# Optimization experiments

Measured on AMD Instinct MI355X. Metric: run time of the kernel, lower is better.

## Reference

```python
import jax, jax.numpy as jnp
import numpy as np
import math
from jax import lax

BATCH, SEQ_LEN, ENC_IN = 8, 2048, 1
D_MODEL, N_HEADS, E_LAYERS, D_FF, FACTOR, C_OUT = 512, 8, 3, 512, 5, 2
EPS = 1e-5


def _layernorm(x, g, b):
    mu = x.mean(-1, keepdims=True)
    var = ((x - mu) ** 2).mean(-1, keepdims=True)
    return (x - mu) / jnp.sqrt(var + EPS) * g + b


def _prob_attention(q, k, v, key):
    # q,k,v: [B,H,L,Dh]; ProbSparse: sample U keys per query, pick top-u queries by M = max - mean
    B, H, L, Dh = q.shape
    U = min(FACTOR * int(np.ceil(np.log(L))), L)  # U_part == u since L_Q == L_K
    idx = jax.random.randint(key, (L, U), 0, L)   # sampled key indices per query
    k_samp = k[:, :, idx, :]                       # [B,H,L,U,Dh]
    qk = jnp.einsum('bhld,bhlud->bhlu', q, k_samp)
    M = qk.max(-1) - qk.mean(-1)                   # sparsity measure [B,H,L]
    _, top = lax.top_k(M, U)                       # active query indices [B,H,U]
    q_red = jnp.take_along_axis(q, top[..., None], axis=2)
    scores = jnp.einsum('bhud,bhkd->bhuk', q_red, k) * (1.0 / math.sqrt(Dh))
    A = jax.nn.softmax(scores, axis=-1)
    ctx = jnp.broadcast_to(v.mean(axis=2, keepdims=True), q.shape)  # lazy-query context = mean(V)
    upd = jnp.einsum('bhuk,bhkd->bhud', A, v)
    b = jnp.arange(B)[:, None, None]
    h = jnp.arange(H)[None, :, None]
    return ctx.at[b, h, top].set(upd)


def _encoder_layer(x, p, key):
    Wq, Wk, Wv, bq, bk, bv, Wo, bo, W1, b1, W2, b2, g1, be1, g2, be2 = p
    B, L, dm = x.shape
    Dh = dm // N_HEADS
    split = lambda t: t.reshape(B, L, N_HEADS, Dh).transpose(0, 2, 1, 3)
    q = split(x @ Wq.T + bq)
    k = split(x @ Wk.T + bk)
    v = split(x @ Wv.T + bv)
    o = _prob_attention(q, k, v, key).transpose(0, 2, 1, 3).reshape(B, L, dm)
    x = _layernorm(x + o @ Wo.T + bo, g1, be1)
    y = jax.nn.gelu(x @ W1.T + b1, approximate=False) @ W2.T + b2  # 1x1 convs == linears
    return _layernorm(x + y, g2, be2)


def _distil_conv(x, w, b, g, be):
    # Conv1d(dm,dm,3, circular pad) -> BatchNorm(eval) -> ELU -> MaxPool1d(3, stride 2, pad 1)
    xc = jnp.pad(x.transpose(0, 2, 1), ((0, 0), (0, 0), (1, 1)), mode='wrap')
    y = lax.conv_general_dilated(xc, w, (1,), 'VALID', dimension_numbers=('NCH', 'OIH', 'NCH'))
    y = y + b[None, :, None]
    y = y / np.float32(np.sqrt(1.0 + EPS)) * g[None, :, None] + be[None, :, None]
    y = jax.nn.elu(y)
    y = lax.reduce_window(y, -jnp.inf, lax.max, (1, 1, 3), (1, 1, 2), [(0, 0), (0, 0), (1, 1)])
    return y.transpose(0, 2, 1)


def _forward(x_enc, tok_w, Wq, Wk, Wv, bq, bk, bv, Wo, bo, W1, b1, W2, b2,
             ln1_g, ln1_b, ln2_g, ln2_b, dc_w, dc_b, bn_g, bn_b, lnf_g, lnf_b, proj_w, proj_b):
    B, L = x_enc.shape
    dm = D_MODEL
    # TokenEmbedding: circular Conv1d(1, d_model, 3, bias=False)
    xc = jnp.pad(x_enc[:, None, :], ((0, 0), (0, 0), (1, 1)), mode='wrap')
    tok = lax.conv_general_dilated(xc, tok_w, (1,), 'VALID', dimension_numbers=('NCH', 'OIH', 'NCH'))
    tok = tok.transpose(0, 2, 1)  # [B,L,dm]
    # fixed sinusoidal positional embedding
    pos = jnp.arange(L, dtype=jnp.float32)[:, None]
    div = jnp.exp(jnp.arange(0, dm, 2, dtype=jnp.float32) * (-math.log(10000.0) / dm))
    pe = jnp.zeros((L, dm), jnp.float32).at[:, 0::2].set(jnp.sin(pos * div)).at[:, 1::2].set(jnp.cos(pos * div))
    x = tok + pe[None]
    key = jax.random.key(42)
    for i in range(E_LAYERS):
        p = (Wq[i], Wk[i], Wv[i], bq[i], bk[i], bv[i], Wo[i], bo[i],
             W1[i], b1[i], W2[i], b2[i], ln1_g[i], ln1_b[i], ln2_g[i], ln2_b[i])
        x = _encoder_layer(x, p, jax.random.fold_in(key, i))
        if i < E_LAYERS - 1:
            x = _distil_conv(x, dc_w[i], dc_b[i], bn_g[i], bn_b[i])
    x = _layernorm(x, lnf_g, lnf_b)
    return x.max(axis=1) @ proj_w.T + proj_b  # [B, C_OUT]


def setup_inputs() -> dict:
    key = jax.random.key(0)
    ks = jax.random.split(key, 12)
    dm, dff, L = D_MODEL, D_FF, E_LAYERS
    w = lambda k, shape, fan: jax.random.normal(k, shape, jnp.float32) / np.float32(np.sqrt(fan))
    return {
        'x_enc': jax.random.normal(ks[0], (BATCH, SEQ_LEN), jnp.float32),
        'tok_w': w(ks[1], (dm, ENC_IN, 3), 3 * ENC_IN),
        'Wq': w(ks[2], (L, dm, dm), dm), 'Wk': w(ks[3], (L, dm, dm), dm),
        'Wv': w(ks[4], (L, dm, dm), dm), 'Wo': w(ks[5], (L, dm, dm), dm),
        'bq': jnp.zeros((L, dm)), 'bk': jnp.zeros((L, dm)),
        'bv': jnp.zeros((L, dm)), 'bo': jnp.zeros((L, dm)),
        'W1': w(ks[6], (L, dff, dm), dm), 'b1': jnp.zeros((L, dff)),
        'W2': w(ks[7], (L, dm, dff), dff), 'b2': jnp.zeros((L, dm)),
        'ln1_g': jnp.ones((L, dm)), 'ln1_b': jnp.zeros((L, dm)),
        'ln2_g': jnp.ones((L, dm)), 'ln2_b': jnp.zeros((L, dm)),
        'dc_w': w(ks[8], (L - 1, dm, dm, 3), 3 * dm), 'dc_b': jnp.zeros((L - 1, dm)),
        'bn_g': jnp.ones((L - 1, dm)), 'bn_b': jnp.zeros((L - 1, dm)),
        'lnf_g': jnp.ones((dm,)), 'lnf_b': jnp.zeros((dm,)),
        'proj_w': w(ks[9], (C_OUT, dm), dm), 'proj_b': jnp.zeros((C_OUT,)),
    }


def reference(x_enc, tok_w, Wq, Wk, Wv, bq, bk, bv, Wo, bo, W1, b1, W2, b2,
              ln1_g, ln1_b, ln2_g, ln2_b, dc_w, dc_b, bn_g, bn_b, lnf_g, lnf_b, proj_w, proj_b):
    return _forward(x_enc, tok_w, Wq, Wk, Wv, bq, bk, bv, Wo, bo, W1, b1, W2, b2,
                    ln1_g, ln1_b, ln2_g, ln2_b, dc_w, dc_b, bn_g, bn_b, lnf_g, lnf_b, proj_w, proj_b)
```

## Files before the change

### kernel.cpp

```cpp
#include <hip/hip_runtime.h>

#define B_ 8
#define H_ 8
#define DM 512
#define DH 64
#define LMAX 2048
#define COUT 2

typedef __attribute__((ext_vector_type(8))) short frag8;
typedef __attribute__((ext_vector_type(4))) float f32x4;

typedef __attribute__((address_space(1))) const unsigned int guint;
typedef __attribute__((address_space(3))) unsigned int luint;
__device__ __forceinline__ void dma16(const short* g, short* l) {
  __builtin_amdgcn_global_load_lds((guint*)g, (luint*)l, 16, 0, 0);
}

__device__ __forceinline__ short f2bf(float v) {
  unsigned u = __float_as_uint(v);
  unsigned r = (u + 0x7fffu + ((u >> 16) & 1u)) >> 16;
  return (short)r;
}
__device__ __forceinline__ float bf2f(short s) {
  return __uint_as_float(((unsigned)(unsigned short)s) << 16);
}
__device__ __forceinline__ void split3(float v, short* p0, short* p1, short* p2, size_t i) {
  short h0 = f2bf(v);
  float r1 = v - bf2f(h0);
  short h1 = f2bf(r1);
  float r2 = r1 - bf2f(h1);
  p0[i] = h0; p1[i] = h1; p2[i] = f2bf(r2);
}

__device__ __forceinline__ void tf2x32(unsigned k0, unsigned k1, unsigned x0, unsigned x1,
                                       unsigned& o0, unsigned& o1) {
  unsigned ks2 = k0 ^ k1 ^ 0x1BD11BDAu;
  x0 += k0; x1 += k1;
#define RND(r) { x0 += x1; x1 = (x1 << r) | (x1 >> (32 - r)); x1 ^= x0; }
  RND(13) RND(15) RND(26) RND(6)  x0 += k1;  x1 += ks2 + 1u;
  RND(17) RND(29) RND(16) RND(24) x0 += ks2; x1 += k0 + 2u;
  RND(13) RND(15) RND(26) RND(6)  x0 += k0;  x1 += k1 + 3u;
  RND(17) RND(29) RND(16) RND(24) x0 += k1;  x1 += ks2 + 4u;
  RND(13) RND(15) RND(26) RND(6)  x0 += ks2; x1 += k0 + 5u;
#undef RND
  o0 = x0; o1 = x1;
}

__global__ void idx_kernel(int* __restrict__ idxArr, int L, int U, int layer) {
  int p = blockIdx.x * 256 + threadIdx.x;
  int half = L * U;
  if (p >= half) return;
  unsigned fk0, fk1, k20, k21, o0, o1;
  tf2x32(0u, 42u, 0u, (unsigned)layer, fk0, fk1);
  tf2x32(fk0, fk1, 0u, 1u, k20, k21);
  tf2x32(k20, k21, 0u, (unsigned)p, o0, o1);
  idxArr[p] = (int)((o0 ^ o1) & (unsigned)(L - 1));
}

__global__ void embed_kernel(const float* __restrict__ xe, const float* __restrict__ tw,
                             float* __restrict__ X, short* __restrict__ P0,
                             short* __restrict__ P1, short* __restrict__ P2) {
  int i = blockIdx.x * 256 + threadIdx.x;
  int c = i % DM;
  int l = (i / DM) % LMAX;
  int b = i / (DM * LMAX);
  int lm = (l + LMAX - 1) & (LMAX - 1);
  int lp = (l + 1) & (LMAX - 1);
  const float* xb = xe + b * LMAX;
  float tok = tw[c * 3 + 0] * xb[lm] + tw[c * 3 + 1] * xb[l] + tw[c * 3 + 2] * xb[lp];
  float freq = expf(-(float)(c & ~1) * (9.210340371976184f / 512.0f));
  float ang = (float)l * freq;
  float pe = (c & 1) ? cosf(ang) : sinf(ang);
  float v = tok + pe;
  X[i] = v;
  split3(v, P0, P1, P2, (size_t)i);
}

__global__ void wsplit_kernel(const float* __restrict__ W, short* __restrict__ P0,
                              short* __restrict__ P1, short* __restrict__ P2, int n) {
  int i = blockIdx.x * 256 + threadIdx.x;
  if (i >= n) return;
  split3(W[i], P0, P1, P2, (size_t)i);
}

__global__ void wt3_kernel(const float* __restrict__ w, short* __restrict__ P0,
                           short* __restrict__ P1, short* __restrict__ P2) {
  int i = blockIdx.x * 256 + threadIdx.x;
  int n = i / 1536, r = i - n * 1536, tap = r >> 9, k = r & 511;
  float v = w[((size_t)n * DM + k) * 3 + tap];
  split3(v, P0, P1, P2, (size_t)i);
}

template <int ACT, int QKV, int ACC, int CONV>
__global__ __launch_bounds__(256) void mgemm(const short* __restrict__ A0g,
                                             const short* __restrict__ A1g,
                                             const short* __restrict__ A2g,
                                             const short* __restrict__ W0g,
                                             const short* __restrict__ W1g,
                                             const short* __restrict__ W2g,
                                             const float* __restrict__ bias,
                                             float* __restrict__ C, int L, int Ktot) {
  __shared__ short A0[128 * 32], A1[128 * 32], A2[128 * 32];
  __shared__ short B0[128 * 32], B1[128 * 32], B2[128 * 32];
  int tid = threadIdx.x;
  int lane = tid & 63, wave = tid >> 6;
  int crow = lane >> 2, ckq = lane & 3;
  int gx = gridDim.x;
  int flat = blockIdx.y * gx + blockIdx.x;
  int mB, nB;
  if ((gridDim.y & 7) == 0) {
    int phase = flat & 7, sup = flat >> 3;
    nB = sup % gx;
    mB = phase + 8 * (sup / gx);
  } else {
    nB = blockIdx.x; mB = blockIdx.y;
  }
  int n0 = nB * 128, m0 = mB * 128;
  int wm = (wave >> 1) * 64, wn = (wave & 1) * 64;
  f32x4 acc[4][4] = {};
  int lrow = lane & 15, lq = lane >> 4;

  for (int k0 = 0; k0 < Ktot; k0 += 32) {
    int tap = 0, kcol = k0;
    if (CONV) { tap = k0 >> 9; kcol = k0 & 511; }
#pragma unroll
    for (int q = 0; q < 6; ++q) {
      int gc = wave * 6 + q;
      int pl = gc >> 3, c = gc & 7;
      int grow = m0 + c * 16 + crow;
      const short* gp;
      if (CONV) {
        int b = grow / L, l = grow - b * L;
        int le = l + tap - 1;
        le = (le < 0) ? le + L : (le >= L ? le - L : le);
        gp = ((size_t)(b * L + le) * DM + kcol + ckq * 8) +
             (pl == 0 ? A0g : pl == 1 ? A1g : A2g);
      } else {
        gp = ((size_t)grow * DM + k0 + ckq * 8) +
             (pl == 0 ? A0g : pl == 1 ? A1g : A2g);
      }
      short* lp = (pl == 0 ? A0 : pl == 1 ? A1 : A2) + c * 512;
      dma16(gp, lp);
    }
#pragma unroll
    for (int q = 0; q < 6; ++q) {
      int gc = wave * 6 + q;
      int pl = gc >> 3, c = gc & 7;
      int grow = n0 + c * 16 + crow;
      const short* gp = ((size_t)grow * Ktot + k0 + ckq * 8) +
                        (pl == 0 ? W0g : pl == 1 ? W1g : W2g);
      short* lp = (pl == 0 ? B0 : pl == 1 ? B1 : B2) + c * 512;
      dma16(gp, lp);
    }
    __syncthreads();
    frag8 a0f[4], a1f[4], a2f[4];
#pragma unroll
    for (int ti = 0; ti < 4; ++ti) {
      int off = (wm + ti * 16 + lrow) * 32 + lq * 8;
      a0f[ti] = *(const frag8*)&A0[off];
      a1f[ti] = *(const frag8*)&A1[off];
      a2f[ti] = *(const frag8*)&A2[off];
    }
#pragma unroll
    for (int tj = 0; tj < 4; ++tj) {
      int off = (wn + tj * 16 + lrow) * 32 + lq * 8;
      frag8 b0 = *(const frag8*)&B0[off];
      frag8 b1 = *(const frag8*)&B1[off];
      frag8 b2 = *(const frag8*)&B2[off];
#pragma unroll
      for (int ti = 0; ti < 4; ++ti) {
        f32x4 ac = acc[ti][tj];
        ac = __builtin_amdgcn_mfma_f32_16x16x32_bf16(a1f[ti], b1, ac, 0, 0, 0);
        ac = __builtin_amdgcn_mfma_f32_16x16x32_bf16(a0f[ti], b2, ac, 0, 0, 0);
        ac = __builtin_amdgcn_mfma_f32_16x16x32_bf16(a2f[ti], b0, ac, 0, 0, 0);
        ac = __builtin_amdgcn_mfma_f32_16x16x32_bf16(a0f[ti], b1, ac, 0, 0, 0);
        ac = __builtin_amdgcn_mfma_f32_16x16x32_bf16(a1f[ti], b0, ac, 0, 0, 0);
        ac = __builtin_amdgcn_mfma_f32_16x16x32_bf16(a0f[ti], b0, ac, 0, 0, 0);
        acc[ti][tj] = ac;
      }
    }
    __syncthreads();
  }
#pragma unroll
  for (int ti = 0; ti < 4; ++ti) {
#pragma unroll
    for (int tj = 0; tj < 4; ++tj) {
#pragma unroll
      for (int r = 0; r < 4; ++r) {
        int row = m0 + wm + ti * 16 + lq * 4 + r;
        int col = n0 + wn + tj * 16 + lrow;
        float v = acc[ti][tj][r];
        if (!CONV) v += bias[col];
        if (ACT) v = 0.5f * v * (1.0f + erff(v * 0.70710678118654752f));
        if (QKV) {
          int b = row / L, l = row - b * L;
          int h = col >> 6, d = col & 63;
          C[(((size_t)b * H_ + h) * L + l) * DH + d] = v;
        } else if (ACC) {
          C[(size_t)row * DM + col] += v;
        } else {
          C[(size_t)row * DM + col] = v;
        }
      }
    }
  }
}

__global__ void bnelu_kernel(float* __restrict__ Y, const float* __restrict__ cb,
                             const float* __restrict__ g, const float* __restrict__ be) {
  int i = blockIdx.x * 256 + threadIdx.x;
  int c = i % DM;
  const float invs = 0.9999950000374997f;
  float z = Y[i] + cb[c];
  z = z * invs * g[c] + be[c];
  Y[i] = z > 0.f ? z : expm1f(z);
}

template <int U>
__global__ void qkM_t(const float* __restrict__ Q, const float* __restrict__ Kd,
                      const int* __restrict__ idxArr, float* __restrict__ Mout, int L) {
  int lane = threadIdx.x & 63, wv = threadIdx.x >> 6;
  int row = blockIdx.x * 4 + wv;
  int l = row % L, bh = row / L;
  int u = lane & 7, dc = lane >> 3;
  const float* Qb = Q + ((size_t)bh * L + l) * DH + dc * 8;
  float4 q0 = *(const float4*)(Qb);
  float4 q1 = *(const float4*)(Qb + 4);
  const float* Kb = Kd + (size_t)bh * L * DH;
  const int* ip = idxArr + l * U;
  const int NP = (U + 7) / 8;
  float mx = -1e30f, sm = 0.f;
#pragma unroll
  for (int p = 0; p < NP; ++p) {
    int s = p * 8 + u;
    bool valid = (s < U);
    int ki = ip[valid ? s : 0];
    const float* kr = Kb + (size_t)ki * DH + dc * 8;
    float4 k0 = *(const float4*)(kr);
    float4 k1 = *(const float4*)(kr + 4);
    float d = q0.x * k0.x + q0.y * k0.y + q0.z * k0.z + q0.w * k0.w +
              q1.x * k1.x + q1.y * k1.y + q1.z * k1.z + q1.w * k1.w;
    d += __shfl_xor(d, 8, 64);
    d += __shfl_xor(d, 16, 64);
    d += __shfl_xor(d, 32, 64);
    if (valid) { mx = fmaxf(mx, d); sm += d; }
  }
#pragma unroll
  for (int o = 1; o <= 4; o <<= 1) {
    mx = fmaxf(mx, __shfl_xor(mx, o, 64));
    sm += __shfl_xor(sm, o, 64);
  }
  if (lane == 0) Mout[row] = mx - sm / (float)U;
}

__global__ void topk_kernel(const float* __restrict__ M, int* __restrict__ top, int L, int U) {
  __shared__ float vals[LMAX];
  __shared__ float rv[256];
  __shared__ int ri[256];
  int bh = blockIdx.x, tid = threadIdx.x;
  for (int j = tid; j < L; j += 256) vals[j] = M[(size_t)bh * L + j];
  __syncthreads();
  for (int u = 0; u < U; ++u) {
    float bv = -1e30f; int bi = L;
    for (int j = tid; j < L; j += 256) {
      float v = vals[j];
      if (v > bv) { bv = v; bi = j; }
    }
    rv[tid] = bv; ri[tid] = bi;
    __syncthreads();
    for (int s = 128; s >= 1; s >>= 1) {
      if (tid < s) {
        float ov = rv[tid + s]; int oi = ri[tid + s];
        if (ov > rv[tid] || (ov == rv[tid] && oi < ri[tid])) { rv[tid] = ov; ri[tid] = oi; }
      }
      __syncthreads();
    }
    if (tid == 0) { top[bh * U + u] = ri[0]; vals[ri[0]] = -1e30f; }
    __syncthreads();
  }
}

__global__ void vmean_kernel(const float* __restrict__ V, float* __restrict__ VM, int L) {
  __shared__ float red[256];
  int bh = blockIdx.x, tid = threadIdx.x, d = tid & 63, sq = tid >> 6;
  float s = 0.f;
  for (int l = sq; l < L; l += 4) s += V[((size_t)bh * L + l) * DH + d];
  red[tid] = s;
  __syncthreads();
  if (sq == 0) VM[bh * DH + d] = (red[d] + red[d + 64] + red[d + 128] + red[d + 192]) / (float)L;
}

__global__ void fill_kernel(const float* __restrict__ VM, short* __restrict__ P0,
                            short* __restrict__ P1, short* __restrict__ P2, int L) {
  size_t i = (size_t)blockIdx.x * 256 + threadIdx.x;
  int c = (int)(i % DM);
  int b = (int)(i / ((size_t)L * DM));
  split3(VM[b * DM + c], P0, P1, P2, i);
}

__global__ __launch_bounds__(512) void attn_fused(const float* __restrict__ Q,
                                                  const float* __restrict__ Kd,
                                                  const float* __restrict__ V,
                                                  const int* __restrict__ top,
                                                  short* __restrict__ OP0,
                                                  short* __restrict__ OP1,
                                                  short* __restrict__ OP2,
                                                  int L, int U) {
  __shared__ float Qs[8][64];
  __shared__ float Kt[64][65];
  __shared__ float Vs[64][68];
  __shared__ float ps[8][64];
  __shared__ int lst[8];
  int nch = (U + 7) >> 3;
  int bh = blockIdx.x / nch, ch = blockIdx.x - bh * nch;
  int u0g = ch * 8;
  int qn = U - u0g; if (qn > 8) qn = 8;
  int tid = threadIdx.x, lane = tid & 63, wv = tid >> 6;
  if (tid < qn) lst[tid] = top[bh * U + u0g + tid];
  __syncthreads();
  if (tid < qn * 64) {
    int u = tid >> 6, d = tid & 63;
    Qs[u][d] = Q[((size_t)bh * L + lst[u]) * DH + d];
  }
  __syncthreads();
  int ua = wv;
  bool hasA = ua < qn;
  float m0 = -1e30f, l0 = 0.f, o0 = 0.f;
  const float* Kbase = Kd + (size_t)bh * L * DH;
  const float* Vbase = V + (size_t)bh * L * DH;
  for (int t0 = 0; t0 < L; t0 += 64) {
#pragma unroll
    for (int it = 0; it < 2; ++it) {
      int idx = tid + it * 512;
      int j = idx >> 4, d4 = (idx & 15) * 4;
      float4 kv = *(const float4*)(Kbase + (size_t)(t0 + j) * DH + d4);
      Kt[d4 + 0][j] = kv.x; Kt[d4 + 1][j] = kv.y;
      Kt[d4 + 2][j] = kv.z; Kt[d4 + 3][j] = kv.w;
      *(float4*)&Vs[j][d4] = *(const float4*)(Vbase + (size_t)(t0 + j) * DH + d4);
    }
    __syncthreads();
    float s0 = 0.f;
#pragma unroll 16
    for (int d = 0; d < 64; ++d) {
      float kd = Kt[d][lane];
      s0 += kd * Qs[ua & 7][d];
    }
    s0 *= 0.125f;
    if (hasA) {
      float tm = s0;
#pragma unroll
      for (int o = 32; o >= 1; o >>= 1) tm = fmaxf(tm, __shfl_xor(tm, o, 64));
      float nm = fmaxf(m0, tm);
      float alpha = expf(m0 - nm);
      float p = expf(s0 - nm);
      float tsum = p;
#pragma unroll
      for (int o = 32; o >= 1; o >>= 1) tsum += __shfl_xor(tsum, o, 64);
      l0 = l0 * alpha + tsum;
      m0 = nm;
      ps[ua][lane] = p;
      o0 *= alpha;
#pragma unroll 16
      for (int j = 0; j < 64; ++j) o0 += ps[ua][j] * Vs[j][lane];
    }
    __syncthreads();
  }
  int b = bh / H_, h = bh - b * H_;
  if (hasA) {
    size_t i = ((size_t)b * L + lst[ua]) * DM + h * DH + lane;
    split3(o0 / l0, OP0, OP1, OP2, i);
  }
}

__global__ void ln_kernel(float* __restrict__ X, const float* __restrict__ g,
                          const float* __restrict__ be, short* __restrict__ P0,
                          short* __restrict__ P1, short* __restrict__ P2) {
  __shared__ float red[256];
  int row = blockIdx.x, tid = threadIdx.x;
  size_t base = (size_t)row * DM;
  float t0 = X[base + tid];
  float t1 = X[base + tid + 256];
  red[tid] = t0 + t1;
  __syncthreads();
  for (int s = 128; s >= 1; s >>= 1) { if (tid < s) red[tid] += red[tid + s]; __syncthreads(); }
  float mu = red[0] / 512.0f;
  __syncthreads();
  float d0 = t0 - mu, d1 = t1 - mu;
  red[tid] = d0 * d0 + d1 * d1;
  __syncthreads();
  for (int s = 128; s >= 1; s >>= 1) { if (tid < s) red[tid] += red[tid + s]; __syncthreads(); }
  float rstd = 1.0f / sqrtf(red[0] / 512.0f + 1e-5f);
  float v0 = d0 * rstd * g[tid] + be[tid];
  float v1 = d1 * rstd * g[tid + 256] + be[tid + 256];
  X[base + tid] = v0;
  X[base + tid + 256] = v1;
  if (P0) {
    split3(v0, P0, P1, P2, base + tid);
    split3(v1, P0, P1, P2, base + tid + 256);
  }
}

__global__ void pool_kernel(const float* __restrict__ Y, float* __restrict__ X, int L2,
                            short* __restrict__ P0, short* __restrict__ P1,
                            short* __restrict__ P2) {
  int i = blockIdx.x * 256 + threadIdx.x;
  int c = i % DM;
  int t = (i / DM) % L2;
  int b = i / (DM * L2);
  int L = L2 * 2;
  const float* yb = Y + (size_t)b * L * DM + c;
  float m = fmaxf(yb[(size_t)(2 * t) * DM], yb[(size_t)(2 * t + 1) * DM]);
  if (t > 0) m = fmaxf(m, yb[(size_t)(2 * t - 1) * DM]);
  X[i] = m;
  split3(m, P0, P1, P2, (size_t)i);
}

__global__ void colmax1_kernel(const float* __restrict__ X, float* __restrict__ P, int L) {
  int nlc = L >> 6;
  int bl = blockIdx.x;
  int b = bl / nlc, lc = bl % nlc;
  const float* xb = X + ((size_t)b * L + lc * 64) * DM;
  for (int c = threadIdx.x; c < DM; c += 256) {
    float m = -1e30f;
    for (int r = 0; r < 64; ++r) m = fmaxf(m, xb[(size_t)r * DM + c]);
    P[((size_t)b * nlc + lc) * DM + c] = m;
  }
}
__global__ void colmax2_kernel(const float* __restrict__ P, float* __restrict__ mc, int nlc) {
  int i = blockIdx.x * 256 + threadIdx.x;
  int b = i / DM, c = i % DM;
  float m = -1e30f;
  for (int lc = 0; lc < nlc; ++lc) m = fmaxf(m, P[((size_t)b * nlc + lc) * DM + c]);
  mc[i] = m;
}

__global__ void proj_kernel(const float* __restrict__ mc, const float* __restrict__ pw,
                            const float* __restrict__ pb, float* __restrict__ out) {
  __shared__ float red[256];
  int bo = blockIdx.x, b = bo / COUT, o = bo % COUT, tid = threadIdx.x;
  float s = mc[b * DM + tid] * pw[o * DM + tid] +
            mc[b * DM + tid + 256] * pw[o * DM + tid + 256];
  red[tid] = s;
  __syncthreads();
  for (int st = 128; st >= 1; st >>= 1) { if (tid < st) red[tid] += red[tid + st]; __syncthreads(); }
  if (tid == 0) out[bo] = red[0] + pb[o];
}

extern "C" void kernel_launch(void* const* d_in, const int* in_sizes, int n_in,
                              void* d_out, int out_size, void* d_ws, size_t ws_size,
                              hipStream_t stream) {
  (void)in_sizes; (void)n_in; (void)out_size;
  const float* xe   = (const float*)d_in[0];
  const float* tw   = (const float*)d_in[1];
  const float* Wq   = (const float*)d_in[2];
  const float* Wk   = (const float*)d_in[3];
  const float* Wv   = (const float*)d_in[4];
  const float* Wo   = (const float*)d_in[5];
  const float* bq   = (const float*)d_in[6];
  const float* bk   = (const float*)d_in[7];
  const float* bv   = (const float*)d_in[8];
  const float* bo   = (const float*)d_in[9];
  const float* W1   = (const float*)d_in[10];
  const float* b1   = (const float*)d_in[11];
  const float* W2   = (const float*)d_in[12];
  const float* b2   = (const float*)d_in[13];
  const float* ln1g = (const float*)d_in[14];
  const float* ln1b = (const float*)d_in[15];
  const float* ln2g = (const float*)d_in[16];
  const float* ln2b = (const float*)d_in[17];
  const float* dcw  = (const float*)d_in[18];
  const float* dcb  = (const float*)d_in[19];
  const float* bng  = (const float*)d_in[20];
  const float* bnb  = (const float*)d_in[21];
  const float* lnfg = (const float*)d_in[22];
  const float* lnfb = (const float*)d_in[23];
  const float* pw   = (const float*)d_in[24];
  const float* pb   = (const float*)d_in[25];
  float* out = (float*)d_out;

  float* Wf = (float*)d_ws;
  const size_t NB  = (size_t)B_ * LMAX * DM;
  const size_t NHB = (size_t)H_ * LMAX * DH;
  const size_t S_IDX = 81920, S_MV = 131072, S_TOP = 4096, S_VM = 4096,
               S_MC = 4096, S_P = 32768;
  const size_t PLANE  = (size_t)512 * 1536;
  const size_t APLANE = NB;
  const size_t S_WP = 3 * PLANE / 2 + 1024;
  const size_t S_AP = 3 * APLANE / 2 + 1024;
  const size_t SMALL = S_IDX + S_MV + S_TOP + S_VM + S_MC + S_P + S_WP + S_AP + 1024;

  int g = 8;
  while (g > 1 && (2 * NB + 3 * (size_t)g * NHB + SMALL) * 4 > ws_size) g >>= 1;

  float* X  = Wf;
  float* T  = X + NB;
  float* Q  = T + NB;
  float* K  = Q + (size_t)g * NHB;
  float* V  = K + (size_t)g * NHB;
  float* SM = V + (size_t)g * NHB;
  int*   IDX = (int*)SM;
  float* Mv  = SM + S_IDX;
  int*   TOP = (int*)(Mv + S_MV);
  float* VM  = Mv + S_MV + S_TOP;
  float* MC  = VM + S_VM;
  float* P   = MC + S_MC;
  short* WP0 = (short*)(P + S_P);
  short* WP1 = WP0 + PLANE;
  short* WP2 = WP1 + PLANE;
  short* AP0 = (short*)((float*)(P + S_P) + S_WP);
  short* AP1 = AP0 + APLANE;
  short* AP2 = AP1 + APLANE;

  embed_kernel<<<B_ * LMAX * DM / 256, 256, 0, stream>>>(xe, tw, X, AP0, AP1, AP2);

  int L = LMAX;
  for (int i = 0; i < 3; ++i) {
    int U = (i == 0) ? 40 : 35;
    size_t wOff = (size_t)i * DM * DM;
    int ng = B_ / g;
    int nch = (U + 7) >> 3;
    const int NW = DM * DM;

    idx_kernel<<<(L * U + 255) / 256, 256, 0, stream>>>(IDX, L, U, i);

    for (int gb = 0; gb < ng; ++gb) {
      size_t aoff = (size_t)gb * g * L * DM;
      dim3 gq(DM / 128, g * L / 128);
      wsplit_kernel<<<NW / 256, 256, 0, stream>>>(Wq + wOff, WP0, WP1, WP2, NW);
      mgemm<0, 1, 0, 0><<<gq, 256, 0, stream>>>(AP0 + aoff, AP1 + aoff, AP2 + aoff,
                                                WP0, WP1, WP2, bq + i * DM, Q, L, DM);
      wsplit_kernel<<<NW / 256, 256, 0, stream>>>(Wk + wOff, WP0, WP1, WP2, NW);
      mgemm<0, 1, 0, 0><<<gq, 256, 0, stream>>>(AP0 + aoff, AP1 + aoff, AP2 + aoff,
                                                WP0, WP1, WP2, bk + i * DM, K, L, DM);
      wsplit_kernel<<<NW / 256, 256, 0, stream>>>(Wv + wOff, WP0, WP1, WP2, NW);
      mgemm<0, 1, 0, 0><<<gq, 256, 0, stream>>>(AP0 + aoff, AP1 + aoff, AP2 + aoff,
                                                WP0, WP1, WP2, bv + i * DM, V, L, DM);
      if (U == 40) qkM_t<40><<<g * H_ * L / 4, 256, 0, stream>>>(Q, K, IDX, Mv, L);
      else         qkM_t<35><<<g * H_ * L / 4, 256, 0, stream>>>(Q, K, IDX, Mv, L);
      topk_kernel<<<g * H_, 256, 0, stream>>>(Mv, TOP, L, U);
      vmean_kernel<<<g * H_, 256, 0, stream>>>(V, VM, L);
      fill_kernel<<<(unsigned)((size_t)g * L * DM / 256), 256, 0, stream>>>(
          VM, AP0 + aoff, AP1 + aoff, AP2 + aoff, L);
      attn_fused<<<g * H_ * nch, 512, 0, stream>>>(Q, K, V, TOP, AP0 + aoff,
                                                   AP1 + aoff, AP2 + aoff, L, U);
    }

    int Mf = B_ * L * DM;
    dim3 gf(DM / 128, B_ * L / 128);
    wsplit_kernel<<<NW / 256, 256, 0, stream>>>(Wo + wOff, WP0, WP1, WP2, NW);
    mgemm<0, 0, 1, 0><<<gf, 256, 0, stream>>>(AP0, AP1, AP2, WP0, WP1, WP2,
                                              bo + i * DM, X, L, DM);
    ln_kernel<<<B_ * L, 256, 0, stream>>>(X, ln1g + i * DM, ln1b + i * DM, AP0, AP1, AP2);
    wsplit_kernel<<<NW / 256, 256, 0, stream>>>(W1 + wOff, WP0, WP1, WP2, NW);
    mgemm<1, 0, 0, 0><<<gf, 256, 0, stream>>>(AP0, AP1, AP2, WP0, WP1, WP2,
                                              b1 + i * DM, T, L, DM);
    wsplit_kernel<<<Mf / 256, 256, 0, stream>>>(T, AP0, AP1, AP2, Mf);
    wsplit_kernel<<<NW / 256, 256, 0, stream>>>(W2 + wOff, WP0, WP1, WP2, NW);
    mgemm<0, 0, 1, 0><<<gf, 256, 0, stream>>>(AP0, AP1, AP2, WP0, WP1, WP2,
                                              b2 + i * DM, X, L, DM);
    if (i < 2) {
      ln_kernel<<<B_ * L, 256, 0, stream>>>(X, ln2g + i * DM, ln2b + i * DM, AP0, AP1, AP2);
      wt3_kernel<<<DM * 1536 / 256, 256, 0, stream>>>(dcw + (size_t)i * DM * DM * 3,
                                                      WP0, WP1, WP2);
      mgemm<0, 0, 0, 1><<<gf, 256, 0, stream>>>(AP0, AP1, AP2, WP0, WP1, WP2,
                                                nullptr, T, L, 1536);
      bnelu_kernel<<<B_ * L * DM / 256, 256, 0, stream>>>(T, dcb + i * DM, bng + i * DM,
                                                          bnb + i * DM);
      L >>= 1;
      pool_kernel<<<B_ * L * DM / 256, 256, 0, stream>>>(T, X, L, AP0, AP1, AP2);
    } else {
      ln_kernel<<<B_ * L, 256, 0, stream>>>(X, ln2g + i * DM, ln2b + i * DM,
                                            nullptr, nullptr, nullptr);
    }
  }

  ln_kernel<<<B_ * L, 256, 0, stream>>>(X, lnfg, lnfb, nullptr, nullptr, nullptr);
  colmax1_kernel<<<B_ * (L >> 6), 256, 0, stream>>>(X, P, L);
  colmax2_kernel<<<B_ * DM / 256, 256, 0, stream>>>(P, MC, L >> 6);
  proj_kernel<<<B_ * COUT, 256, 0, stream>>>(MC, pw, pb, out);
}
```

Measured before the change: 2.280 ms.

## Fuse QKV GEMMs, fold BN+ELU into conv epilogue, warp-shuffle topk

```diff
diff --git a/kernel.cpp b/kernel.cpp
--- a/kernel.cpp
+++ b/kernel.cpp
@@ -91,7 +91,13 @@
   split3(v, P0, P1, P2, (size_t)i);
 }
 
-template <int ACT, int QKV, int ACC, int CONV>
+__global__ void bcat_kernel(const float* __restrict__ bq, const float* __restrict__ bk,
+                            const float* __restrict__ bv, float* __restrict__ o) {
+  int i = blockIdx.x * 256 + threadIdx.x;
+  o[i] = i < 512 ? bq[i] : (i < 1024 ? bk[i - 512] : bv[i - 1024]);
+}
+
+template <int ACT, int QKV, int ACC, int CONV, int BN>
 __global__ __launch_bounds__(256) void mgemm(const short* __restrict__ A0g,
                                              const short* __restrict__ A1g,
                                              const short* __restrict__ A2g,
@@ -99,7 +105,10 @@
                                              const short* __restrict__ W1g,
                                              const short* __restrict__ W2g,
                                              const float* __restrict__ bias,
-                                             float* __restrict__ C, int L, int Ktot) {
+                                             const float* __restrict__ bng,
+                                             const float* __restrict__ bnbe,
+                                             float* __restrict__ C, long qs,
+                                             int L, int Ktot) {
   __shared__ short A0[128 * 32], A1[128 * 32], A2[128 * 32];
   __shared__ short B0[128 * 32], B1[128 * 32], B2[128 * 32];
   int tid = threadIdx.x;
@@ -192,10 +201,17 @@
         float v = acc[ti][tj][r];
         if (!CONV) v += bias[col];
         if (ACT) v = 0.5f * v * (1.0f + erff(v * 0.70710678118654752f));
+        if (BN) {
+          const float invs = 0.9999950000374997f;
+          float z = v + bias[col];
+          z = z * invs * bng[col] + bnbe[col];
+          v = z > 0.f ? z : expm1f(z);
+        }
         if (QKV) {
+          int sel = col >> 9, cc = col & 511;
           int b = row / L, l = row - b * L;
-          int h = col >> 6, d = col & 63;
-          C[(((size_t)b * H_ + h) * L + l) * DH + d] = v;
+          int h = cc >> 6, d = cc & 63;
+          C[(size_t)sel * qs + (((size_t)b * H_ + h) * L + l) * DH + d] = v;
         } else if (ACC) {
           C[(size_t)row * DM + col] += v;
         } else {
@@ -204,16 +220,6 @@
       }
     }
   }
-}
-
-__global__ void bnelu_kernel(float* __restrict__ Y, const float* __restrict__ cb,
-                             const float* __restrict__ g, const float* __restrict__ be) {
-  int i = blockIdx.x * 256 + threadIdx.x;
-  int c = i % DM;
-  const float invs = 0.9999950000374997f;
-  float z = Y[i] + cb[c];
-  z = z * invs * g[c] + be[c];
-  Y[i] = z > 0.f ? z : expm1f(z);
 }
 
 template <int U>
@@ -255,9 +261,9 @@
 
 __global__ void topk_kernel(const float* __restrict__ M, int* __restrict__ top, int L, int U) {
   __shared__ float vals[LMAX];
-  __shared__ float rv[256];
-  __shared__ int ri[256];
-  int bh = blockIdx.x, tid = threadIdx.x;
+  __shared__ float wvv[4];
+  __shared__ int wii[4];
+  int bh = blockIdx.x, tid = threadIdx.x, lane = tid & 63, w = tid >> 6;
   for (int j = tid; j < L; j += 256) vals[j] = M[(size_t)bh * L + j];
   __syncthreads();
   for (int u = 0; u < U; ++u) {
@@ -266,16 +272,22 @@
       float v = vals[j];
       if (v > bv) { bv = v; bi = j; }
     }
-    rv[tid] = bv; ri[tid] = bi;
+#pragma unroll
+    for (int o = 32; o >= 1; o >>= 1) {
+      float ov = __shfl_xor(bv, o, 64);
+      int oi = __shfl_xor(bi, o, 64);
+      if (ov > bv || (ov == bv && oi < bi)) { bv = ov; bi = oi; }
+    }
+    if (lane == 0) { wvv[w] = bv; wii[w] = bi; }
     __syncthreads();
-    for (int s = 128; s >= 1; s >>= 1) {
-      if (tid < s) {
-        float ov = rv[tid + s]; int oi = ri[tid + s];
-        if (ov > rv[tid] || (ov == rv[tid] && oi < ri[tid])) { rv[tid] = ov; ri[tid] = oi; }
+    if (tid == 0) {
+#pragma unroll
+      for (int k = 1; k < 4; ++k) {
+        if (wvv[k] > bv || (wvv[k] == bv && wii[k] < bi)) { bv = wvv[k]; bi = wii[k]; }
       }
-      __syncthreads();
-    }
-    if (tid == 0) { top[bh * U + u] = ri[0]; vals[ri[0]] = -1e30f; }
+      top[bh * U + u] = bi;
+      vals[bi] = -1e30f;
+    }
     __syncthreads();
   }
 }
@@ -482,12 +494,12 @@
   const size_t NB  = (size_t)B_ * LMAX * DM;
   const size_t NHB = (size_t)H_ * LMAX * DH;
   const size_t S_IDX = 81920, S_MV = 131072, S_TOP = 4096, S_VM = 4096,
-               S_MC = 4096, S_P = 32768;
+               S_MC = 4096, S_BC = 2048, S_P = 32768;
   const size_t PLANE  = (size_t)512 * 1536;
   const size_t APLANE = NB;
   const size_t S_WP = 3 * PLANE / 2 + 1024;
   const size_t S_AP = 3 * APLANE / 2 + 1024;
-  const size_t SMALL = S_IDX + S_MV + S_TOP + S_VM + S_MC + S_P + S_WP + S_AP + 1024;
+  const size_t SMALL = S_IDX + S_MV + S_TOP + S_VM + S_MC + S_BC + S_P + S_WP + S_AP + 1024;
 
   int g = 8;
   while (g > 1 && (2 * NB + 3 * (size_t)g * NHB + SMALL) * 4 > ws_size) g >>= 1;
@@ -503,7 +515,8 @@
   int*   TOP = (int*)(Mv + S_MV);
   float* VM  = Mv + S_MV + S_TOP;
   float* MC  = VM + S_VM;
-  float* P   = MC + S_MC;
+  float* BCAT = MC + S_MC;
+  float* P   = BCAT + S_BC;
   short* WP0 = (short*)(P + S_P);
   short* WP1 = WP0 + PLANE;
   short* WP2 = WP1 + PLANE;
@@ -525,16 +538,16 @@
 
     for (int gb = 0; gb < ng; ++gb) {
       size_t aoff = (size_t)gb * g * L * DM;
-      dim3 gq(DM / 128, g * L / 128);
+      bcat_kernel<<<6, 256, 0, stream>>>(bq + i * DM, bk + i * DM, bv + i * DM, BCAT);
       wsplit_kernel<<<NW / 256, 256, 0, stream>>>(Wq + wOff, WP0, WP1, WP2, NW);
-      mgemm<0, 1, 0, 0><<<gq, 256, 0, stream>>>(AP0 + aoff, AP1 + aoff, AP2 + aoff,
-                                                WP0, WP1, WP2, bq + i * DM, Q, L, DM);
-      wsplit_kernel<<<NW / 256, 256, 0, stream>>>(Wk + wOff, WP0, WP1, WP2, NW);
-      mgemm<0, 1, 0, 0><<<gq, 256, 0, stream>>>(AP0 + aoff, AP1 + aoff, AP2 + aoff,
-                                                WP0, WP1, WP2, bk + i * DM, K, L, DM);
-      wsplit_kernel<<<NW / 256, 256, 0, stream>>>(Wv + wOff, WP0, WP1, WP2, NW);
-      mgemm<0, 1, 0, 0><<<gq, 256, 0, stream>>>(AP0 + aoff, AP1 + aoff, AP2 + aoff,
-                                                WP0, WP1, WP2, bv + i * DM, V, L, DM);
+      wsplit_kernel<<<NW / 256, 256, 0, stream>>>(Wk + wOff, WP0 + NW, WP1 + NW,
+                                                  WP2 + NW, NW);
+      wsplit_kernel<<<NW / 256, 256, 0, stream>>>(Wv + wOff, WP0 + 2 * NW, WP1 + 2 * NW,
+                                                  WP2 + 2 * NW, NW);
+      dim3 gq3(1536 / 128, g * L / 128);
+      mgemm<0, 1, 0, 0, 0><<<gq3, 256, 0, stream>>>(
+          AP0 + aoff, AP1 + aoff, AP2 + aoff, WP0, WP1, WP2, BCAT, nullptr, nullptr,
+          Q, (long)((size_t)g * NHB), L, DM);
       if (U == 40) qkM_t<40><<<g * H_ * L / 4, 256, 0, stream>>>(Q, K, IDX, Mv, L);
       else         qkM_t<35><<<g * H_ * L / 4, 256, 0, stream>>>(Q, K, IDX, Mv, L);
       topk_kernel<<<g * H_, 256, 0, stream>>>(Mv, TOP, L, U);
@@ -548,24 +561,26 @@
     int Mf = B_ * L * DM;
     dim3 gf(DM / 128, B_ * L / 128);
     wsplit_kernel<<<NW / 256, 256, 0, stream>>>(Wo + wOff, WP0, WP1, WP2, NW);
-    mgemm<0, 0, 1, 0><<<gf, 256, 0, stream>>>(AP0, AP1, AP2, WP0, WP1, WP2,
-                                              bo + i * DM, X, L, DM);
+    mgemm<0, 0, 1, 0, 0><<<gf, 256, 0, stream>>>(AP0, AP1, AP2, WP0, WP1, WP2,
+                                                 bo + i * DM, nullptr, nullptr,
+                                                 X, 0, L, DM);
     ln_kernel<<<B_ * L, 256, 0, stream>>>(X, ln1g + i * DM, ln1b + i * DM, AP0, AP1, AP2);
     wsplit_kernel<<<NW / 256, 256, 0, stream>>>(W1 + wOff, WP0, WP1, WP2, NW);
-    mgemm<1, 0, 0, 0><<<gf, 256, 0, stream>>>(AP0, AP1, AP2, WP0, WP1, WP2,
-                                              b1 + i * DM, T, L, DM);
+    mgemm<1, 0, 0, 0, 0><<<gf, 256, 0, stream>>>(AP0, AP1, AP2, WP0, WP1, WP2,
+                                                 b1 + i * DM, nullptr, nullptr,
+                                                 T, 0, L, DM);
     wsplit_kernel<<<Mf / 256, 256, 0, stream>>>(T, AP0, AP1, AP2, Mf);
     wsplit_kernel<<<NW / 256, 256, 0, stream>>>(W2 + wOff, WP0, WP1, WP2, NW);
-    mgemm<0, 0, 1, 0><<<gf, 256, 0, stream>>>(AP0, AP1, AP2, WP0, WP1, WP2,
-                                              b2 + i * DM, X, L, DM);
+    mgemm<0, 0, 1, 0, 0><<<gf, 256, 0, stream>>>(AP0, AP1, AP2, WP0, WP1, WP2,
+                                                 b2 + i * DM, nullptr, nullptr,
+                                                 X, 0, L, DM);
     if (i < 2) {
       ln_kernel<<<B_ * L, 256, 0, stream>>>(X, ln2g + i * DM, ln2b + i * DM, AP0, AP1, AP2);
       wt3_kernel<<<DM * 1536 / 256, 256, 0, stream>>>(dcw + (size_t)i * DM * DM * 3,
                                                       WP0, WP1, WP2);
-      mgemm<0, 0, 0, 1><<<gf, 256, 0, stream>>>(AP0, AP1, AP2, WP0, WP1, WP2,
-                                                nullptr, T, L, 1536);
-      bnelu_kernel<<<B_ * L * DM / 256, 256, 0, stream>>>(T, dcb + i * DM, bng + i * DM,
-                                                          bnb + i * DM);
+      mgemm<0, 0, 0, 1, 1><<<gf, 256, 0, stream>>>(AP0, AP1, AP2, WP0, WP1, WP2,
+                                                   dcb + i * DM, bng + i * DM,
+                                                   bnb + i * DM, T, 0, L, 1536);
       L >>= 1;
       pool_kernel<<<B_ * L * DM / 256, 256, 0, stream>>>(T, X, L, AP0, AP1, AP2);
     } else {
```

Result: faster. 2.167 ms (-5.0%).
